# Performance work log

Hardware: AMD Instinct MI355X
Metric: run time of the kernel (lower is better)

Reference implementation:

```python
import jax, jax.numpy as jnp
import numpy as np

D_MODEL = 512
N_HEADS = 8
D_K = D_MODEL // N_HEADS  # 64
EPS = 1e-5


def setup_inputs() -> dict:
    key = jax.random.key(0)
    ks = jax.random.split(key, 16)
    s = 0.02
    B, T = 4, 2048
    return {
        "x": jax.random.normal(ks[0], (B, T, D_MODEL), dtype=jnp.float32),
        # per-head q/k/v projections stacked over heads: [H, d_model, d_k]
        "Wq": jax.random.normal(ks[1], (N_HEADS, D_MODEL, D_K), dtype=jnp.float32) * s,
        "bq": jnp.zeros((N_HEADS, D_K), dtype=jnp.float32),
        "Wk": jax.random.normal(ks[2], (N_HEADS, D_MODEL, D_K), dtype=jnp.float32) * s,
        "bk": jnp.zeros((N_HEADS, D_K), dtype=jnp.float32),
        "Wv": jax.random.normal(ks[3], (N_HEADS, D_MODEL, D_K), dtype=jnp.float32) * s,
        "bv": jnp.zeros((N_HEADS, D_K), dtype=jnp.float32),
        "Wp": jax.random.normal(ks[4], (D_MODEL, D_MODEL), dtype=jnp.float32) * s,
        "bp": jnp.zeros((D_MODEL,), dtype=jnp.float32),
        "W1": jax.random.normal(ks[5], (D_MODEL, 4 * D_MODEL), dtype=jnp.float32) * s,
        "b1": jnp.zeros((4 * D_MODEL,), dtype=jnp.float32),
        "W2": jax.random.normal(ks[6], (4 * D_MODEL, D_MODEL), dtype=jnp.float32) * s,
        "b2": jnp.zeros((D_MODEL,), dtype=jnp.float32),
        "g1": jnp.ones((D_MODEL,), dtype=jnp.float32),
        "be1": jnp.zeros((D_MODEL,), dtype=jnp.float32),
        "g2": jnp.ones((D_MODEL,), dtype=jnp.float32),
        "be2": jnp.zeros((D_MODEL,), dtype=jnp.float32),
    }


def _layer_norm(x, g, b):
    mu = jnp.mean(x, axis=-1, keepdims=True)
    var = jnp.var(x, axis=-1, keepdims=True)
    return (x - mu) * jax.lax.rsqrt(var + EPS) * g + b


def _block(x, Wq, bq, Wk, bk, Wv, bv, Wp, bp, W1, b1, W2, b2, g1, be1, g2, be2):
    B, T, _ = x.shape
    h = _layer_norm(x, g1, be1)
    # batched per-head projections: [B, H, T, d_k]
    q = jnp.einsum('btd,hdk->bhtk', h, Wq) + bq[:, None, :]
    k = jnp.einsum('btd,hdk->bhtk', h, Wk) + bk[:, None, :]
    v = jnp.einsum('btd,hdk->bhtk', h, Wv) + bv[:, None, :]
    scores = jnp.einsum('bhtk,bhsk->bhts', q, k)  # [B, H, T, T]
    causal = jnp.tril(jnp.ones((T, T), dtype=bool))
    # faithful to source: mask with -1e9 BEFORE dividing by sqrt(d_k)
    scores = jnp.where(causal, scores, jnp.float32(-1e9))
    attn = jax.nn.softmax(scores / jnp.float32(np.sqrt(D_K)), axis=-1)
    o = jnp.einsum('bhts,bhsk->bhtk', attn, v)  # [B, H, T, d_k]
    o = o.transpose(0, 2, 1, 3).reshape(B, T, D_MODEL)  # concat heads
    x = x + o @ Wp + bp
    h2 = _layer_norm(x, g2, be2)
    ff = jax.nn.relu(h2 @ W1 + b1) @ W2 + b2
    return x + ff


def reference(x, Wq, bq, Wk, bk, Wv, bv, Wp, bp, W1, b1, W2, b2, g1, be1, g2, be2):
    return _block(x, Wq, bq, Wk, bk, Wv, bv, Wp, bp, W1, b1, W2, b2, g1, be1, g2, be2)
```

## Files before the change

### kernel.cpp

```cpp
#include <hip/hip_runtime.h>
#include <hip/hip_bf16.h>
#include <math.h>

#define BATCH 4
#define SEQ   2048
#define DM    512
#define NH    8
#define DK    64
#define FF    2048
#define BT    (BATCH * SEQ)

#define SCALE_Q 0.18033688011112042f

typedef short bf16x8 __attribute__((ext_vector_type(8)));
typedef float f32x4  __attribute__((ext_vector_type(4)));

static __device__ inline short f2bf(float f) {
  union { float f; unsigned u; } v; v.f = f;
  unsigned r = (v.u + 0x7fffu + ((v.u >> 16) & 1u)) >> 16;
  return (short)r;
}

static __device__ __forceinline__ void gload16(const short* g, short* l) {
  __builtin_amdgcn_global_load_lds(
      (const __attribute__((address_space(1))) void*)g,
      (__attribute__((address_space(3))) void*)l, 16, 0, 0);
}

static __device__ __forceinline__ void xcd_swizzle(int& bx, int& by) {
  int gx = gridDim.x;
  int nwg = gx * gridDim.y;
  int id = blockIdx.x + gx * blockIdx.y;
  int nid = (id & 7) * (nwg >> 3) + (id >> 3);
  bx = nid % gx;
  by = nid / gx;
}

__global__ __launch_bounds__(256) void ln_kernel(
    const float* __restrict__ x, const float* __restrict__ gamma,
    const float* __restrict__ beta, short* __restrict__ out) {
  int row = blockIdx.x;
  const float* xr = x + (size_t)row * DM;
  int t = threadIdx.x;
  float v0 = xr[t], v1 = xr[t + 256];
  float s = v0 + v1;
  float sq = v0 * v0 + v1 * v1;
  for (int off = 32; off; off >>= 1) {
    s  += __shfl_xor(s, off);
    sq += __shfl_xor(sq, off);
  }
  __shared__ float ssum[4], ssq[4];
  int wave = t >> 6, lane = t & 63;
  if (lane == 0) { ssum[wave] = s; ssq[wave] = sq; }
  __syncthreads();
  if (t == 0) {
    float S = ssum[0] + ssum[1] + ssum[2] + ssum[3];
    float Q = ssq[0] + ssq[1] + ssq[2] + ssq[3];
    float mu = S * (1.0f / DM);
    float var = Q * (1.0f / DM) - mu * mu;
    ssum[0] = mu;
    ssq[0] = rsqrtf(var + 1e-5f);
  }
  __syncthreads();
  float mu = ssum[0], rstd = ssq[0];
  short* orow = out + (size_t)row * DM;
  orow[t]       = f2bf((v0 - mu) * rstd * gamma[t]       + beta[t]);
  orow[t + 256] = f2bf((v1 - mu) * rstd * gamma[t + 256] + beta[t + 256]);
}

__global__ __launch_bounds__(256) void wconv_kernel(
    const float* Wq, const float* Wk, const float* Wv,
    const float* Wp, const float* W1, const float* W2,
    short* wqkv, short* wpt, short* w1t, short* w2t) {
  int z = blockIdx.z;
  const float* src; short* dst; int R, C;
  if (z < 24) {
    int m = z >> 3, hh = z & 7;
    const float* s0 = (m == 0) ? Wq : (m == 1) ? Wk : Wv;
    src = s0 + (size_t)hh * 512 * 64;
    dst = wqkv + ((size_t)(m * 512 + hh * 64)) * 512;
    R = 512; C = 64;
  } else if (z == 24) { src = Wp; dst = wpt; R = 512;  C = 512;  }
  else if (z == 25)   { src = W1; dst = w1t; R = 512;  C = 2048; }
  else                { src = W2; dst = w2t; R = 2048; C = 512;  }
  int tx = blockIdx.x, ty = blockIdx.y;
  if (tx >= C / 64 || ty >= R / 64) return;
  __shared__ float Ts[64][68];
  int t = threadIdx.x;
  int r = t >> 2, c0 = (t & 3) * 16;
  const float* sp = src + (size_t)(ty * 64 + r) * C + tx * 64 + c0;
#pragma unroll
  for (int i = 0; i < 16; i += 4) {
    float4 v = *(const float4*)(sp + i);
    Ts[c0 + i + 0][r] = v.x; Ts[c0 + i + 1][r] = v.y;
    Ts[c0 + i + 2][r] = v.z; Ts[c0 + i + 3][r] = v.w;
  }
  __syncthreads();
  short* dp = dst + (size_t)(tx * 64 + r) * R + ty * 64 + c0;
  short tmp[16];
#pragma unroll
  for (int i = 0; i < 16; ++i) tmp[i] = f2bf(Ts[r][c0 + i]);
  *(int4*)(dp)     = *(int4*)&tmp[0];
  *(int4*)(dp + 8) = *(int4*)&tmp[8];
}

template<int TM, int TN>
__device__ __forceinline__ void gemm_core(
    const short* __restrict__ A, const short* __restrict__ Bw,
    int m0, int n0, int K, short* smem, f32x4 (&acc)[TM / 32][TN / 32]) {
  constexpr int AF = TM / 32, BF = TN / 32;
  constexpr int AC = TM / 64, BC = TN / 64;
  constexpr int BUFS = (TM + TN) * 32;
  int t = threadIdx.x;
  int wave = t >> 6, lane = t & 63, quad = lane >> 4, l16 = lane & 15;
  int wr = wave >> 1, wc = wave & 1;

  size_t aoff[AC], boff[BC];
  int aldsoff[AC], bldsoff[BC];
#pragma unroll
  for (int c = 0; c < AC; ++c) {
    int p = c * 256 + t, row = p >> 2, lg = (p & 3) ^ ((row >> 1) & 3);
    aoff[c] = (size_t)(m0 + row) * K + lg * 8;
    aldsoff[c] = c * 2048 + wave * 512;
  }
#pragma unroll
  for (int c = 0; c < BC; ++c) {
    int p = c * 256 + t, row = p >> 2, lg = (p & 3) ^ ((row >> 1) & 3);
    boff[c] = (size_t)(n0 + row) * K + lg * 8;
    bldsoff[c] = TM * 32 + c * 2048 + wave * 512;
  }

#pragma unroll
  for (int c = 0; c < AC; ++c) gload16(A + aoff[c], smem + aldsoff[c]);
#pragma unroll
  for (int c = 0; c < BC; ++c) gload16(Bw + boff[c], smem + bldsoff[c]);

  int physo = (quad ^ ((l16 >> 1) & 3)) * 8;

  for (int k0 = 0; k0 < K; k0 += 32) {
    short* cbuf = smem + ((k0 >> 5) & 1) * BUFS;
    __syncthreads();
    if (k0 + 32 < K) {
      short* nbuf = smem + (((k0 >> 5) & 1) ^ 1) * BUFS;
#pragma unroll
      for (int c = 0; c < AC; ++c) gload16(A + aoff[c] + k0 + 32, nbuf + aldsoff[c]);
#pragma unroll
      for (int c = 0; c < BC; ++c) gload16(Bw + boff[c] + k0 + 32, nbuf + bldsoff[c]);
    }
    bf16x8 af[AF], bfr[BF];
#pragma unroll
    for (int i = 0; i < AF; ++i)
      af[i] = *(const bf16x8*)&cbuf[(wr * (TM / 2) + i * 16 + l16) * 32 + physo];
#pragma unroll
    for (int j = 0; j < BF; ++j)
      bfr[j] = *(const bf16x8*)&cbuf[TM * 32 + (wc * (TN / 2) + j * 16 + l16) * 32 + physo];
#pragma unroll
    for (int i = 0; i < AF; ++i)
#pragma unroll
      for (int j = 0; j < BF; ++j)
        acc[i][j] = __builtin_amdgcn_mfma_f32_16x16x32_bf16(bfr[j], af[i], acc[i][j], 0, 0, 0);
  }
}

template<int TM, int TN>
__global__ __launch_bounds__(256) void mgemm_kernel(
    const short* __restrict__ A, const short* __restrict__ Bw,
    const float* __restrict__ bias, const float* __restrict__ res,
    void* __restrict__ C, int N, int K, int dorelu, int bf16out) {
  __shared__ __align__(16) short smem[(TM + TN) * 64];
  f32x4 acc[TM / 32][TN / 32];
  f32x4 zf = {0.f, 0.f, 0.f, 0.f};
#pragma unroll
  for (int i = 0; i < TM / 32; ++i)
#pragma unroll
    for (int j = 0; j < TN / 32; ++j) acc[i][j] = zf;
  int bx, by;
  xcd_swizzle(bx, by);
  int m0 = by * TM, n0 = bx * TN;
  gemm_core<TM, TN>(A, Bw, m0, n0, K, smem, acc);

  int t = threadIdx.x;
  int wave = t >> 6, lane = t & 63, quad = lane >> 4, l16 = lane & 15;
  int wr = wave >> 1, wc = wave & 1;
#pragma unroll
  for (int i = 0; i < TM / 32; ++i) {
    int m = m0 + wr * (TM / 2) + i * 16 + l16;
#pragma unroll
    for (int j = 0; j < TN / 32; ++j) {
      int nb = n0 + wc * (TN / 2) + j * 16 + quad * 4;
      float4 bv = *(const float4*)&bias[nb];
      float v[4] = {acc[i][j][0] + bv.x, acc[i][j][1] + bv.y,
                    acc[i][j][2] + bv.z, acc[i][j][3] + bv.w};
      if (dorelu) {
#pragma unroll
        for (int r = 0; r < 4; ++r) v[r] = fmaxf(v[r], 0.0f);
      }
      size_t off = (size_t)m * N + nb;
      if (res) {
        float4 rv = *(const float4*)(res + off);
        v[0] += rv.x; v[1] += rv.y; v[2] += rv.z; v[3] += rv.w;
      }
      if (bf16out) {
        short tmp[4] = {f2bf(v[0]), f2bf(v[1]), f2bf(v[2]), f2bf(v[3])};
        *(int2*)((short*)C + off) = *(int2*)tmp;
      } else {
        float4 outv = {v[0], v[1], v[2], v[3]};
        *(float4*)((float*)C + off) = outv;
      }
    }
  }
}

__global__ __launch_bounds__(256) void qkv_kernel(
    const short* __restrict__ A, const short* __restrict__ Bw,
    const float* __restrict__ bq, const float* __restrict__ bk,
    const float* __restrict__ bv,
    short* __restrict__ q, short* __restrict__ k, short* __restrict__ vt) {
  __shared__ __align__(16) short smem[17408];
  f32x4 acc[4][4];
  f32x4 zf = {0.f, 0.f, 0.f, 0.f};
#pragma unroll
  for (int i = 0; i < 4; ++i)
#pragma unroll
    for (int j = 0; j < 4; ++j) acc[i][j] = zf;
  int bx, by;
  xcd_swizzle(bx, by);
  int m0 = by * 128, n0 = bx * 128;
  gemm_core<128, 128>(A, Bw, m0, n0, DM, smem, acc);

  int t = threadIdx.x;
  int wave = t >> 6, lane = t & 63, quad = lane >> 4, l16 = lane & 15;
  int wr = wave >> 1, wc = wave & 1;

  if (n0 < 1024) {
    short* out = (n0 < 512) ? q : k;
    const float* bias = (n0 < 512) ? bq + n0 : bk + (n0 - 512);
    float scale = (n0 < 512) ? SCALE_Q : 1.0f;
    int ncol0 = (n0 < 512) ? n0 : n0 - 512;
#pragma unroll
    for (int i = 0; i < 4; ++i) {
      int m = m0 + wr * 64 + i * 16 + l16;
#pragma unroll
      for (int j = 0; j < 4; ++j) {
        int nb = wc * 64 + j * 16 + quad * 4;
        float4 bvv = *(const float4*)&bias[nb];
        short tmp[4];
        tmp[0] = f2bf((acc[i][j][0] + bvv.x) * scale);
        tmp[1] = f2bf((acc[i][j][1] + bvv.y) * scale);
        tmp[2] = f2bf((acc[i][j][2] + bvv.z) * scale);
        tmp[3] = f2bf((acc[i][j][3] + bvv.w) * scale);
        *(int2*)(out + (size_t)m * DM + ncol0 + nb) = *(int2*)tmp;
      }
    }
  } else {
    const float* bias = bv + (n0 - 1024);
    __syncthreads();
    short* Ts = smem;
#pragma unroll
    for (int i = 0; i < 4; ++i) {
      int ml = wr * 64 + i * 16 + l16;
#pragma unroll
      for (int j = 0; j < 4; ++j) {
        int nb = wc * 64 + j * 16 + quad * 4;
        float4 bvv = *(const float4*)&bias[nb];
        Ts[(nb + 0) * 136 + ml] = f2bf(acc[i][j][0] + bvv.x);
        Ts[(nb + 1) * 136 + ml] = f2bf(acc[i][j][1] + bvv.y);
        Ts[(nb + 2) * 136 + ml] = f2bf(acc[i][j][2] + bvv.z);
        Ts[(nb + 3) * 136 + ml] = f2bf(acc[i][j][3] + bvv.w);
      }
    }
    __syncthreads();
    int nl = t >> 1, half = (t & 1) * 64;
    int gn = (n0 - 1024) + nl;
    int hh = gn >> 6, dk = gn & 63;
    int bidx = m0 >> 11, s0 = (m0 & 2047) + half;
    short* dst = vt + ((size_t)((bidx * NH + hh) * DK + dk)) * SEQ + s0;
    const short* srcT = &Ts[nl * 136 + half];
#pragma unroll
    for (int i2 = 0; i2 < 64; i2 += 8)
      *(int4*)(dst + i2) = *(const int4*)(srcT + i2);
  }
}

template<bool DIAG>
static __device__ __forceinline__ void attn_tile(
    const short* __restrict__ KsC, const short* __restrict__ VsC,
    short* __restrict__ Psw, const bf16x8& qf0, const bf16x8& qf1,
    f32x4 (&o_acc)[4], float& l_part, int quad, int l16,
    int keyb0, int qrow) {
  f32x4 zf = {0.f, 0.f, 0.f, 0.f};
  int sw = l16 & 7;

#pragma unroll
  for (int nt = 0; nt < 4; ++nt) {
    int krow = nt * 16 + l16;
    bf16x8 ka0 = *(const bf16x8*)&KsC[krow * 64 + ((quad ^ sw) * 8)];
    bf16x8 ka1 = *(const bf16x8*)&KsC[krow * 64 + (((4 + quad) ^ sw) * 8)];
    f32x4 s = __builtin_amdgcn_mfma_f32_16x16x32_bf16(ka0, qf0, zf, 0, 0, 0);
    s = __builtin_amdgcn_mfma_f32_16x16x32_bf16(ka1, qf1, s, 0, 0, 0);
    float pr[4];
#pragma unroll
    for (int r = 0; r < 4; ++r) {
      float e = exp2f(s[r]);
      if (DIAG) {
        int key = keyb0 + nt * 16 + quad * 4 + r;
        e = (key > qrow) ? 0.0f : e;
      }
      pr[r] = e;
      l_part += e;
    }
    unsigned pk0 = __builtin_amdgcn_perm(
        __float_as_uint(pr[1]), __float_as_uint(pr[0]), 0x07060302u);
    unsigned pk1 = __builtin_amdgcn_perm(
        __float_as_uint(pr[3]), __float_as_uint(pr[2]), 0x07060302u);
    int2 w = {(int)pk0, (int)pk1};
    *(int2*)&Psw[l16 * 72 + nt * 16 + quad * 4] = w;
  }

  bf16x8 apf0 = *(const bf16x8*)&Psw[l16 * 72 + quad * 8];
  bf16x8 apf1 = *(const bf16x8*)&Psw[l16 * 72 + 32 + quad * 8];
  __builtin_amdgcn_s_setprio(1);
#pragma unroll
  for (int nt2 = 0; nt2 < 4; ++nt2) {
    int vrow = nt2 * 16 + l16;
    bf16x8 vf0 = *(const bf16x8*)&VsC[vrow * 64 + ((quad ^ sw) * 8)];
    bf16x8 vf1 = *(const bf16x8*)&VsC[vrow * 64 + (((4 + quad) ^ sw) * 8)];
    o_acc[nt2] = __builtin_amdgcn_mfma_f32_16x16x32_bf16(vf0, apf0, o_acc[nt2], 0, 0, 0);
    o_acc[nt2] = __builtin_amdgcn_mfma_f32_16x16x32_bf16(vf1, apf1, o_acc[nt2], 0, 0, 0);
  }
  __builtin_amdgcn_s_setprio(0);
}

__global__ __launch_bounds__(256) void fattn_kernel(
    const short* __restrict__ Q, const short* __restrict__ Kg,
    const short* __restrict__ Vt, short* __restrict__ O) {
  int id = blockIdx.x + 32 * (blockIdx.y + NH * blockIdx.z);
  int c = id & 7, j = id >> 3;
  int g = c * 4 + (j & 3);
  int qt = 31 - (j >> 2);
  int h = g & 7, b = g >> 3;
  int q0 = qt * 64;
  int t = threadIdx.x, wave = t >> 6, lane = t & 63, quad = lane >> 4, l16 = lane & 15;

  __shared__ __align__(16) short Ks[2][64 * 64];
  __shared__ __align__(16) short Vs[2][64 * 64];
  __shared__ __align__(16) short Ps[4][16 * 72];

  f32x4 zf = {0.f, 0.f, 0.f, 0.f};
  const short* qp = Q + ((size_t)(b * SEQ + q0 + wave * 16 + l16)) * DM + h * DK;
  bf16x8 qf0 = *(const bf16x8*)(qp + quad * 8);
  bf16x8 qf1 = *(const bf16x8*)(qp + 32 + quad * 8);

  f32x4 o_acc[4];
  float l_part = 0.0f;
#pragma unroll
  for (int i = 0; i < 4; ++i) o_acc[i] = zf;

  const short* kb = Kg + ((size_t)(b * SEQ)) * DM + h * DK;
  const short* vb = Vt + ((size_t)((b * NH + h) * DK)) * SEQ;

  int row0 = t >> 3,         lg0 = (t & 7) ^ (row0 & 7);
  int row1 = (256 + t) >> 3, lg1 = ((256 + t) & 7) ^ (row1 & 7);
  const short* kp0 = kb + (size_t)row0 * DM + lg0 * 8;
  const short* kp1 = kb + (size_t)row1 * DM + lg1 * 8;
  const short* vp0 = vb + (size_t)row0 * SEQ + lg0 * 8;
  const short* vp1 = vb + (size_t)row1 * SEQ + lg1 * 8;
  int lo0 = wave * 512, lo1 = 2048 + wave * 512;

  gload16(kp0, &Ks[0][lo0]); gload16(kp1, &Ks[0][lo1]);
  gload16(vp0, &Vs[0][lo0]); gload16(vp1, &Vs[0][lo1]);
  kp0 += 64 * DM; kp1 += 64 * DM; vp0 += 64; vp1 += 64;

  int qrow = q0 + wave * 16 + l16;
  short* Psw = &Ps[wave][0];

  int buf = 0;
  for (int kt = 0; kt < qt; ++kt) {
    __syncthreads();
    int nb = buf ^ 1;
    gload16(kp0, &Ks[nb][lo0]); gload16(kp1, &Ks[nb][lo1]);
    gload16(vp0, &Vs[nb][lo0]); gload16(vp1, &Vs[nb][lo1]);
    kp0 += 64 * DM; kp1 += 64 * DM; vp0 += 64; vp1 += 64;
    attn_tile<false>(&Ks[buf][0], &Vs[buf][0], Psw, qf0, qf1,
                     o_acc, l_part, quad, l16, 0, qrow);
    buf = nb;
  }
  __syncthreads();
  attn_tile<true>(&Ks[buf][0], &Vs[buf][0], Psw, qf0, qf1,
                  o_acc, l_part, quad, l16, qt * 64, qrow);

  float lf = l_part;
  lf += __shfl_xor(lf, 16);
  lf += __shfl_xor(lf, 32);
  float inv = 1.0f / lf;
  short* orow = O + ((size_t)(b * SEQ) + qrow) * DM + h * DK;
#pragma unroll
  for (int nt2 = 0; nt2 < 4; ++nt2) {
    short tmp[4];
#pragma unroll
    for (int r = 0; r < 4; ++r) tmp[r] = f2bf(o_acc[nt2][r] * inv);
    *(int2*)(orow + nt2 * 16 + quad * 4) = *(int2*)tmp;
  }
}

extern "C" void kernel_launch(void* const* d_in, const int* in_sizes, int n_in,
                              void* d_out, int out_size, void* d_ws, size_t ws_size,
                              hipStream_t stream) {
  const float* x   = (const float*)d_in[0];
  const float* Wq  = (const float*)d_in[1];
  const float* bq  = (const float*)d_in[2];
  const float* Wk  = (const float*)d_in[3];
  const float* bk  = (const float*)d_in[4];
  const float* Wv  = (const float*)d_in[5];
  const float* bv  = (const float*)d_in[6];
  const float* Wp  = (const float*)d_in[7];
  const float* bp  = (const float*)d_in[8];
  const float* W1  = (const float*)d_in[9];
  const float* b1  = (const float*)d_in[10];
  const float* W2  = (const float*)d_in[11];
  const float* b2  = (const float*)d_in[12];
  const float* g1  = (const float*)d_in[13];
  const float* be1 = (const float*)d_in[14];
  const float* g2  = (const float*)d_in[15];
  const float* be2 = (const float*)d_in[16];
  float* out = (float*)d_out;

  char* wsb = (char*)d_ws;
  const size_t SB = (size_t)BT * DM * 2;
  short* h    = (short*)(wsb);
  short* q    = (short*)(wsb + SB);
  short* k    = (short*)(wsb + 2 * SB);
  short* vt   = (short*)(wsb + 3 * SB);
  short* o    = (short*)(wsb + 4 * SB);
  float* x2   = (float*)(wsb + 5 * SB);
  short* h2   = (short*)(wsb + 5 * SB + (size_t)BT * DM * 4);
  short* ff   = (short*)(wsb + 6 * SB + (size_t)BT * DM * 4);
  short* wqkv = (short*)(wsb + 6 * SB + (size_t)BT * DM * 4 + (size_t)BT * FF * 2);
  short* wpt  = wqkv + 1536 * 512;
  short* w1t  = wpt + 512 * 512;
  short* w2t  = w1t + 2048 * 512;

  dim3 blk(256);

  wconv_kernel<<<dim3(32, 32, 27), blk, 0, stream>>>(Wq, Wk, Wv, Wp, W1, W2,
                                                     wqkv, wpt, w1t, w2t);
  ln_kernel<<<BT, blk, 0, stream>>>(x, g1, be1, h);

  qkv_kernel<<<dim3(12, 64), blk, 0, stream>>>(h, wqkv, bq, bk, bv, q, k, vt);

  fattn_kernel<<<dim3(32, NH, BATCH), blk, 0, stream>>>(q, k, vt, o);

  mgemm_kernel<64, 64><<<dim3(8, 128), blk, 0, stream>>>(o, wpt, bp, x, x2, DM, DM, 0, 0);
  ln_kernel<<<BT, blk, 0, stream>>>(x2, g2, be2, h2);
  mgemm_kernel<128, 128><<<dim3(16, 64), blk, 0, stream>>>(h2, w1t, b1, nullptr, ff, FF, DM, 1, 1);
  mgemm_kernel<64, 64><<<dim3(8, 128), blk, 0, stream>>>(ff, w2t, b2, x2, out, DM, FF, 0, 0);
}
```

Baseline: 267.6 us.

## Process 128 query rows per attention block to reuse K/V tiles across two row groups

Each wave now handles two 16-row query groups (32 rows) instead of one, so a block covers 128 query rows and each staged 64-key K/V tile feeds twice as many MFMAs. This halves the grid and the K/V global traffic per query, and amortizes LDS loads of K and V fragments. The cost is more registers per thread (doubled accumulators and Q fragments), a larger P scratch in LDS, and two diagonal tiles at the end of each block. Fewer blocks (512) may reduce load balance or occupancy on the causal schedule.

Result: slower. 283.8 us (+6.0%).

```diff
diff --git a/kernel.cpp b/kernel.cpp
--- a/kernel.cpp
+++ b/kernel.cpp
@@ -283,11 +283,11 @@
 }
 
 template<bool DIAG>
-static __device__ __forceinline__ void attn_tile(
+static __device__ __forceinline__ void attn_tile2(
     const short* __restrict__ KsC, const short* __restrict__ VsC,
-    short* __restrict__ Psw, const bf16x8& qf0, const bf16x8& qf1,
-    f32x4 (&o_acc)[4], float& l_part, int quad, int l16,
-    int keyb0, int qrow) {
+    short* __restrict__ Psw, const bf16x8 (&qf)[2][2],
+    f32x4 (&o_acc)[2][4], float (&lp)[2], int quad, int l16,
+    int keyb0, int qrow0, int qrow1) {
   f32x4 zf = {0.f, 0.f, 0.f, 0.f};
   int sw = l16 & 7;
 
@@ -296,37 +296,52 @@
     int krow = nt * 16 + l16;
     bf16x8 ka0 = *(const bf16x8*)&KsC[krow * 64 + ((quad ^ sw) * 8)];
     bf16x8 ka1 = *(const bf16x8*)&KsC[krow * 64 + (((4 + quad) ^ sw) * 8)];
-    f32x4 s = __builtin_amdgcn_mfma_f32_16x16x32_bf16(ka0, qf0, zf, 0, 0, 0);
-    s = __builtin_amdgcn_mfma_f32_16x16x32_bf16(ka1, qf1, s, 0, 0, 0);
-    float pr[4];
+    f32x4 s0 = __builtin_amdgcn_mfma_f32_16x16x32_bf16(ka0, qf[0][0], zf, 0, 0, 0);
+    s0 = __builtin_amdgcn_mfma_f32_16x16x32_bf16(ka1, qf[0][1], s0, 0, 0, 0);
+    f32x4 s1 = __builtin_amdgcn_mfma_f32_16x16x32_bf16(ka0, qf[1][0], zf, 0, 0, 0);
+    s1 = __builtin_amdgcn_mfma_f32_16x16x32_bf16(ka1, qf[1][1], s1, 0, 0, 0);
+    int keyq = keyb0 + nt * 16 + quad * 4;
+    float p0[4], p1[4];
 #pragma unroll
     for (int r = 0; r < 4; ++r) {
-      float e = exp2f(s[r]);
-      if (DIAG) {
-        int key = keyb0 + nt * 16 + quad * 4 + r;
-        e = (key > qrow) ? 0.0f : e;
-      }
-      pr[r] = e;
-      l_part += e;
-    }
-    unsigned pk0 = __builtin_amdgcn_perm(
-        __float_as_uint(pr[1]), __float_as_uint(pr[0]), 0x07060302u);
-    unsigned pk1 = __builtin_amdgcn_perm(
-        __float_as_uint(pr[3]), __float_as_uint(pr[2]), 0x07060302u);
-    int2 w = {(int)pk0, (int)pk1};
-    *(int2*)&Psw[l16 * 72 + nt * 16 + quad * 4] = w;
-  }
-
-  bf16x8 apf0 = *(const bf16x8*)&Psw[l16 * 72 + quad * 8];
-  bf16x8 apf1 = *(const bf16x8*)&Psw[l16 * 72 + 32 + quad * 8];
+      float e = exp2f(s0[r]);
+      p0[r] = (DIAG && (keyq + r > qrow0)) ? 0.0f : e;
+    }
+    lp[0] += (p0[0] + p0[1]) + (p0[2] + p0[3]);
+#pragma unroll
+    for (int r = 0; r < 4; ++r) {
+      float e = exp2f(s1[r]);
+      p1[r] = (DIAG && (keyq + r > qrow1)) ? 0.0f : e;
+    }
+    lp[1] += (p1[0] + p1[1]) + (p1[2] + p1[3]);
+    unsigned a0 = __builtin_amdgcn_perm(
+        __float_as_uint(p0[1]), __float_as_uint(p0[0]), 0x07060302u);
+    unsigned a1 = __builtin_amdgcn_perm(
+        __float_as_uint(p0[3]), __float_as_uint(p0[2]), 0x07060302u);
+    int2 w0 = {(int)a0, (int)a1};
+    *(int2*)&Psw[l16 * 72 + nt * 16 + quad * 4] = w0;
+    unsigned b0 = __builtin_amdgcn_perm(
+        __float_as_uint(p1[1]), __float_as_uint(p1[0]), 0x07060302u);
+    unsigned b1 = __builtin_amdgcn_perm(
+        __float_as_uint(p1[3]), __float_as_uint(p1[2]), 0x07060302u);
+    int2 w1 = {(int)b0, (int)b1};
+    *(int2*)&Psw[(16 + l16) * 72 + nt * 16 + quad * 4] = w1;
+  }
+
+  bf16x8 ap00 = *(const bf16x8*)&Psw[l16 * 72 + quad * 8];
+  bf16x8 ap01 = *(const bf16x8*)&Psw[l16 * 72 + 32 + quad * 8];
+  bf16x8 ap10 = *(const bf16x8*)&Psw[(16 + l16) * 72 + quad * 8];
+  bf16x8 ap11 = *(const bf16x8*)&Psw[(16 + l16) * 72 + 32 + quad * 8];
   __builtin_amdgcn_s_setprio(1);
 #pragma unroll
   for (int nt2 = 0; nt2 < 4; ++nt2) {
     int vrow = nt2 * 16 + l16;
     bf16x8 vf0 = *(const bf16x8*)&VsC[vrow * 64 + ((quad ^ sw) * 8)];
     bf16x8 vf1 = *(const bf16x8*)&VsC[vrow * 64 + (((4 + quad) ^ sw) * 8)];
-    o_acc[nt2] = __builtin_amdgcn_mfma_f32_16x16x32_bf16(vf0, apf0, o_acc[nt2], 0, 0, 0);
-    o_acc[nt2] = __builtin_amdgcn_mfma_f32_16x16x32_bf16(vf1, apf1, o_acc[nt2], 0, 0, 0);
+    o_acc[0][nt2] = __builtin_amdgcn_mfma_f32_16x16x32_bf16(vf0, ap00, o_acc[0][nt2], 0, 0, 0);
+    o_acc[0][nt2] = __builtin_amdgcn_mfma_f32_16x16x32_bf16(vf1, ap01, o_acc[0][nt2], 0, 0, 0);
+    o_acc[1][nt2] = __builtin_amdgcn_mfma_f32_16x16x32_bf16(vf0, ap10, o_acc[1][nt2], 0, 0, 0);
+    o_acc[1][nt2] = __builtin_amdgcn_mfma_f32_16x16x32_bf16(vf1, ap11, o_acc[1][nt2], 0, 0, 0);
   }
   __builtin_amdgcn_s_setprio(0);
 }
@@ -334,27 +349,36 @@
 __global__ __launch_bounds__(256) void fattn_kernel(
     const short* __restrict__ Q, const short* __restrict__ Kg,
     const short* __restrict__ Vt, short* __restrict__ O) {
-  int id = blockIdx.x + 32 * (blockIdx.y + NH * blockIdx.z);
+  int id = blockIdx.x + 16 * (blockIdx.y + NH * blockIdx.z);
   int c = id & 7, j = id >> 3;
   int g = c * 4 + (j & 3);
-  int qt = 31 - (j >> 2);
+  int qts = 15 - (j >> 2);
   int h = g & 7, b = g >> 3;
-  int q0 = qt * 64;
+  int q0 = qts * 128;
+  int NT = 2 * qts + 2;
   int t = threadIdx.x, wave = t >> 6, lane = t & 63, quad = lane >> 4, l16 = lane & 15;
 
   __shared__ __align__(16) short Ks[2][64 * 64];
   __shared__ __align__(16) short Vs[2][64 * 64];
-  __shared__ __align__(16) short Ps[4][16 * 72];
+  __shared__ __align__(16) short Ps[4][32 * 72];
 
   f32x4 zf = {0.f, 0.f, 0.f, 0.f};
-  const short* qp = Q + ((size_t)(b * SEQ + q0 + wave * 16 + l16)) * DM + h * DK;
-  bf16x8 qf0 = *(const bf16x8*)(qp + quad * 8);
-  bf16x8 qf1 = *(const bf16x8*)(qp + 32 + quad * 8);
-
-  f32x4 o_acc[4];
-  float l_part = 0.0f;
-#pragma unroll
-  for (int i = 0; i < 4; ++i) o_acc[i] = zf;
+  int qrow0 = q0 + wave * 32 + l16;
+  int qrow1 = qrow0 + 16;
+  const short* qp0 = Q + ((size_t)(b * SEQ + qrow0)) * DM + h * DK;
+  const short* qp1 = Q + ((size_t)(b * SEQ + qrow1)) * DM + h * DK;
+  bf16x8 qf[2][2];
+  qf[0][0] = *(const bf16x8*)(qp0 + quad * 8);
+  qf[0][1] = *(const bf16x8*)(qp0 + 32 + quad * 8);
+  qf[1][0] = *(const bf16x8*)(qp1 + quad * 8);
+  qf[1][1] = *(const bf16x8*)(qp1 + 32 + quad * 8);
+
+  f32x4 o_acc[2][4];
+  float lp[2] = {0.0f, 0.0f};
+#pragma unroll
+  for (int gi = 0; gi < 2; ++gi)
+#pragma unroll
+    for (int i = 0; i < 4; ++i) o_acc[gi][i] = zf;
 
   const short* kb = Kg + ((size_t)(b * SEQ)) * DM + h * DK;
   const short* vb = Vt + ((size_t)((b * NH + h) * DK)) * SEQ;
@@ -367,40 +391,48 @@
   const short* vp1 = vb + (size_t)row1 * SEQ + lg1 * 8;
   int lo0 = wave * 512, lo1 = 2048 + wave * 512;
 
-  gload16(kp0, &Ks[0][lo0]); gload16(kp1, &Ks[0][lo1]);
-  gload16(vp0, &Vs[0][lo0]); gload16(vp1, &Vs[0][lo1]);
-  kp0 += 64 * DM; kp1 += 64 * DM; vp0 += 64; vp1 += 64;
-
-  int qrow = q0 + wave * 16 + l16;
+#define STAGE_KV(B) do {                                     \
+    gload16(kp0, &Ks[B][lo0]); gload16(kp1, &Ks[B][lo1]);    \
+    gload16(vp0, &Vs[B][lo0]); gload16(vp1, &Vs[B][lo1]);    \
+    kp0 += 64 * DM; kp1 += 64 * DM; vp0 += 64; vp1 += 64; } while (0)
+
+  STAGE_KV(0);
+
   short* Psw = &Ps[wave][0];
-
   int buf = 0;
-  for (int kt = 0; kt < qt; ++kt) {
+  for (int kt = 0; kt < NT - 2; ++kt) {
     __syncthreads();
-    int nb = buf ^ 1;
-    gload16(kp0, &Ks[nb][lo0]); gload16(kp1, &Ks[nb][lo1]);
-    gload16(vp0, &Vs[nb][lo0]); gload16(vp1, &Vs[nb][lo1]);
-    kp0 += 64 * DM; kp1 += 64 * DM; vp0 += 64; vp1 += 64;
-    attn_tile<false>(&Ks[buf][0], &Vs[buf][0], Psw, qf0, qf1,
-                     o_acc, l_part, quad, l16, 0, qrow);
-    buf = nb;
+    STAGE_KV(buf ^ 1);
+    attn_tile2<false>(&Ks[buf][0], &Vs[buf][0], Psw, qf,
+                      o_acc, lp, quad, l16, 0, qrow0, qrow1);
+    buf ^= 1;
   }
   __syncthreads();
-  attn_tile<true>(&Ks[buf][0], &Vs[buf][0], Psw, qf0, qf1,
-                  o_acc, l_part, quad, l16, qt * 64, qrow);
-
-  float lf = l_part;
-  lf += __shfl_xor(lf, 16);
-  lf += __shfl_xor(lf, 32);
-  float inv = 1.0f / lf;
-  short* orow = O + ((size_t)(b * SEQ) + qrow) * DM + h * DK;
-#pragma unroll
-  for (int nt2 = 0; nt2 < 4; ++nt2) {
-    short tmp[4];
-#pragma unroll
-    for (int r = 0; r < 4; ++r) tmp[r] = f2bf(o_acc[nt2][r] * inv);
-    *(int2*)(orow + nt2 * 16 + quad * 4) = *(int2*)tmp;
-  }
+  STAGE_KV(buf ^ 1);
+  attn_tile2<true>(&Ks[buf][0], &Vs[buf][0], Psw, qf,
+                   o_acc, lp, quad, l16, (NT - 2) * 64, qrow0, qrow1);
+  buf ^= 1;
+  __syncthreads();
+  attn_tile2<true>(&Ks[buf][0], &Vs[buf][0], Psw, qf,
+                   o_acc, lp, quad, l16, (NT - 1) * 64, qrow0, qrow1);
+
+#pragma unroll
+  for (int gi = 0; gi < 2; ++gi) {
+    float lf = lp[gi];
+    lf += __shfl_xor(lf, 16);
+    lf += __shfl_xor(lf, 32);
+    float inv = 1.0f / lf;
+    int qrow = (gi == 0) ? qrow0 : qrow1;
+    short* orow = O + ((size_t)(b * SEQ) + qrow) * DM + h * DK;
+#pragma unroll
+    for (int nt2 = 0; nt2 < 4; ++nt2) {
+      short tmp[4];
+#pragma unroll
+      for (int r = 0; r < 4; ++r) tmp[r] = f2bf(o_acc[gi][nt2][r] * inv);
+      *(int2*)(orow + nt2 * 16 + quad * 4) = *(int2*)tmp;
+    }
+  }
+#undef STAGE_KV
 }
 
 extern "C" void kernel_launch(void* const* d_in, const int* in_sizes, int n_in,
@@ -448,7 +480,7 @@
 
   qkv_kernel<<<dim3(12, 64), blk, 0, stream>>>(h, wqkv, bq, bk, bv, q, k, vt);
 
-  fattn_kernel<<<dim3(32, NH, BATCH), blk, 0, stream>>>(q, k, vt, o);
+  fattn_kernel<<<dim3(16, NH, BATCH), blk, 0, stream>>>(q, k, vt, o);
 
   mgemm_kernel<64, 64><<<dim3(8, 128), blk, 0, stream>>>(o, wpt, bp, x, x2, DM, DM, 0, 0);
   ln_kernel<<<BT, blk, 0, stream>>>(x2, g2, be2, h2);
```
